# Performance work log

Measured on AMD Instinct MI355X. Metric: run time of the kernel, lower is better.

The kernel has to match this reference:

```python
import jax, jax.numpy as jnp
import numpy as np

HD = 256          # hidden_dim[0]
KF = 2            # k factor
KD = HD * KF      # 512, bilinear feature dim
L = 2000          # hard-coded sequence length
B = 4
NEG = np.float32(np.finfo(np.float32).min)  # finite min, NOT -inf (matches torch code)
EPS = 1e-5


def _fc(x, V, g, b):
    # weight_norm(Linear, dim=None): W = g * V / ||V||_F, then ReLU
    W = (g / jnp.linalg.norm(V)) * V  # [KD, HD]
    return jax.nn.relu(jnp.einsum('blh,kh->blk', x, W) + b)


def setup_inputs() -> dict:
    key = jax.random.key(0)
    ks = jax.random.split(key, 12)
    X = jax.random.normal(ks[0], (B, L, HD), dtype=jnp.float32)
    Y = jax.random.normal(ks[1], (B, L, HD), dtype=jnp.float32)
    mask1 = jax.random.bernoulli(ks[2], 0.8, (B, L)).astype(jnp.float32)
    mask2 = jax.random.bernoulli(ks[3], 0.8, (B, L)).astype(jnp.float32)
    # Q_net / K_net params (single weight-normed linear each)
    Qv = jax.random.normal(ks[4], (KD, HD), dtype=jnp.float32) * 0.05
    Qg = jnp.asarray(1.0, dtype=jnp.float32)
    Qb = jax.random.normal(ks[5], (KD,), dtype=jnp.float32) * 0.05
    Kv = jax.random.normal(ks[6], (KD, HD), dtype=jnp.float32) * 0.05
    Kg = jnp.asarray(1.0, dtype=jnp.float32)
    Kb = jax.random.normal(ks[7], (KD,), dtype=jnp.float32) * 0.05
    h_mat = jax.random.normal(ks[8], (KD,), dtype=jnp.float32)   # (1,1,KD) squeezed
    h_bias = jax.random.normal(ks[9], (), dtype=jnp.float32)     # (1,1,1) squeezed
    gamma = jnp.ones((KD,), dtype=jnp.float32)                   # BatchNorm1d affine
    beta = jnp.zeros((KD,), dtype=jnp.float32)
    return {"X": X, "Y": Y, "mask1": mask1, "mask2": mask2,
            "Qv": Qv, "Qg": Qg, "Qb": Qb, "Kv": Kv, "Kg": Kg, "Kb": Kb,
            "h_mat": h_mat, "h_bias": h_bias, "gamma": gamma, "beta": beta}


def _masked_softmax(A, m_row):
    # m_row: [B,1,L], broadcasts over axis 1; softmax over dim 1 as in torch
    logits = jnp.where(m_row > 0, A, NEG)
    att = jax.nn.softmax(logits, axis=1)
    return m_row * att


def reference(X, Y, mask1, mask2, Qv, Qg, Qb, Kv, Kg, Kb, h_mat, h_bias, gamma, beta):
    A1_X = _fc(X, Qv, Qg, Qb)  # [B,L,KD]
    A1_Y = _fc(Y, Kv, Kg, Kb)
    A2_Y = _fc(Y, Qv, Qg, Qb)
    A2_X = _fc(X, Kv, Kg, Kb)
    # bilinear co-attention maps [B,L,L]
    A1 = jnp.einsum('bvk,bqk->bvq', A1_X * h_mat, A1_Y) + h_bias
    A2 = jnp.einsum('bqk,bvk->bqv', A2_Y * h_mat, A2_X) + h_bias
    m1r = mask1[:, None, :]  # mask1_attend[b,v,q] = mask1[b,q]
    m2r = mask2[:, None, :]
    alpha = _masked_softmax(A1, m2r)
    logits_X = jnp.einsum('bvq,bqk->bvk', alpha, A1_Y) * mask1[:, :, None]
    beta_att = _masked_softmax(A2, m1r)
    logits_Y = jnp.einsum('bqv,bvk->bqk', beta_att, A2_X) * mask2[:, :, None]
    # AvgPool2d((2000,1)) == mean over sequence dim
    pooled = logits_X.mean(axis=1) + logits_Y.mean(axis=1)  # [B,KD]
    # BatchNorm1d training-mode forward (biased batch stats)
    mu = pooled.mean(axis=0)
    var = pooled.var(axis=0)
    return gamma * (pooled - mu) * jax.lax.rsqrt(var + EPS) + beta
```

## Files before the change

kernel.cpp:

```cpp
#include <hip/hip_runtime.h>

#define NB 4
#define LSEQ 2000
#define HD 256
#define KD 512
#define LPAD 2048
#define SMALL_N 18562

using short8 = __attribute__((ext_vector_type(8))) short;
using f32x4  = __attribute__((ext_vector_type(4))) float;
typedef unsigned short u16;

__device__ __forceinline__ float b2f(u16 u) { return __uint_as_float(((unsigned)u) << 16); }
__device__ __forceinline__ u16 f2b(float f) {
    unsigned u = __float_as_uint(f);
    u += 0x7FFFu + ((u >> 16) & 1u);
    return (u16)(u >> 16);
}
__device__ __forceinline__ bool detect32(const void* gamma) {
    return ((const float*)gamma)[0] == 1.0f;
}
__device__ __forceinline__ void gl_lds16(const u16* g, short* l) {
    __builtin_amdgcn_global_load_lds(
        (const __attribute__((address_space(1))) unsigned int*)g,
        (__attribute__((address_space(3))) unsigned int*)l, 16, 0, 0);
}

__global__ void convert_kernel(const void* X, const void* Y, const void* Qv, const void* Kv,
                               const void* m1, const void* m2, const void* Qb, const void* Kb,
                               const void* hm, const void* Qg, const void* Kg,
                               const void* gamma, const void* beta,
                               u16* __restrict__ Xb, u16* __restrict__ Yb,
                               u16* __restrict__ Qvb, u16* __restrict__ Kvb,
                               float* __restrict__ smallf, float* __restrict__ ssq)
{
    const bool is32 = detect32(gamma);
    const int seg = blockIdx.y;
    if (seg < 4) {
        const void* src = seg == 0 ? X : seg == 1 ? Y : seg == 2 ? Qv : Kv;
        u16* dst = seg == 0 ? Xb : seg == 1 ? Yb : seg == 2 ? Qvb : Kvb;
        const int n = (seg < 2) ? NB * LSEQ * HD : KD * HD;
        const int i0 = (blockIdx.x * 256 + threadIdx.x) * 8;
        if (i0 >= n) return;
        uint4 pack;
        u16* v = (u16*)&pack;
        if (is32) {
            float4 fa = ((const float4*)src)[(i0 >> 2)];
            float4 fb = ((const float4*)src)[(i0 >> 2) + 1];
            v[0] = f2b(fa.x); v[1] = f2b(fa.y); v[2] = f2b(fa.z); v[3] = f2b(fa.w);
            v[4] = f2b(fb.x); v[5] = f2b(fb.y); v[6] = f2b(fb.z); v[7] = f2b(fb.w);
        } else {
            pack = ((const uint4*)src)[i0 >> 3];
        }
        ((uint4*)dst)[i0 >> 3] = pack;
        if (seg >= 2) {
            float s = 0.f;
            #pragma unroll
            for (int j = 0; j < 8; ++j) { float f = b2f(v[j]); s = fmaf(f, f, s); }
            #pragma unroll
            for (int off = 32; off > 0; off >>= 1) s += __shfl_xor(s, off);
            if ((threadIdx.x & 63) == 0) atomicAdd(&ssq[seg - 2], s);
        }
    } else {
        const int i0 = (blockIdx.x * 256 + threadIdx.x) * 4;
        for (int i = i0; i < i0 + 4; ++i) {
            if (i >= SMALL_N) break;
            const void* src; int off;
            if      (i <  8000) { src = m1;    off = i; }
            else if (i < 16000) { src = m2;    off = i - 8000; }
            else if (i < 16512) { src = Qb;    off = i - 16000; }
            else if (i < 17024) { src = Kb;    off = i - 16512; }
            else if (i < 17536) { src = hm;    off = i - 17024; }
            else if (i < 18048) { src = gamma; off = i - 17536; }
            else if (i < 18560) { src = beta;  off = i - 18048; }
            else if (i == 18560) {
                float f = ((const float*)Qg)[0];
                smallf[i] = (f == 1.0f) ? 1.0f : b2f(((const u16*)Qg)[0]);
                continue;
            } else {
                float f = ((const float*)Kg)[0];
                smallf[i] = (f == 1.0f) ? 1.0f : b2f(((const u16*)Kg)[0]);
                continue;
            }
            smallf[i] = is32 ? ((const float*)src)[off] : b2f(((const u16*)src)[off]);
        }
    }
}

__global__ __launch_bounds__(256, 2)
void fc_kernel(const u16* __restrict__ X, const u16* __restrict__ Y,
               const u16* __restrict__ Qv, const u16* __restrict__ Kv,
               const float* __restrict__ Qbf, const float* __restrict__ Kbf,
               const float* __restrict__ hf, const float* __restrict__ gv,
               const float* __restrict__ ssq, u16* __restrict__ fc)
{
    const int mt = blockIdx.x, nt = blockIdx.y, t = blockIdx.z;
    const int b = t >> 2, which = t & 3;
    const u16* In = ((which == 0) | (which == 3)) ? (X + (size_t)b * LSEQ * HD)
                                                  : (Y + (size_t)b * LSEQ * HD);
    const bool isQ = (which == 0) | (which == 2);
    const u16* W      = isQ ? Qv : Kv;
    const float* bias = isQ ? Qbf : Kbf;
    const int j = isQ ? 0 : 1;
    const float s = gv[j] / sqrtf(ssq[j]);
    u16* out = fc + (size_t)t * LSEQ * KD;

    __shared__ __align__(16) short As[2][128 * 32];
    __shared__ __align__(16) short Bs[2][128 * 32];

    const int tid = threadIdx.x;
    const int lane = tid & 63, wave = tid >> 6;
    const int wm = wave >> 1, wn = wave & 1;
    const int quad = lane >> 4, l15 = lane & 15;
    const int sr = tid >> 2, sc = tid & 3;
    const int scz = sc ^ ((sr >> 1) & 3);
    const int m0 = mt * 128, n0 = nt * 128;

    int gm0 = min(m0 + sr, LSEQ - 1), gm1 = min(m0 + sr + 64, LSEQ - 1);
    const u16* pA0 = In + (size_t)gm0 * HD + scz * 8;
    const u16* pA1 = In + (size_t)gm1 * HD + scz * 8;
    const u16* pB0 = W + (size_t)(n0 + sr) * HD + scz * 8;
    const u16* pB1 = W + (size_t)(n0 + sr + 64) * HD + scz * 8;
    const int dof = sr * 32 + sc * 8;

    int aoff[4], boff[4];
    #pragma unroll
    for (int i = 0; i < 4; ++i) {
        int ra = wm * 64 + i * 16 + l15;
        aoff[i] = ra * 32 + (quad ^ ((ra >> 1) & 3)) * 8;
        int rb = wn * 64 + i * 16 + l15;
        boff[i] = rb * 32 + (quad ^ ((rb >> 1) & 3)) * 8;
    }

    gl_lds16(pA0, &As[0][dof]);
    gl_lds16(pA1, &As[0][64 * 32 + dof]);
    gl_lds16(pB0, &Bs[0][dof]);
    gl_lds16(pB1, &Bs[0][64 * 32 + dof]);
    __syncthreads();

    f32x4 acc[4][4] = {};

    for (int kt = 0; kt < 8; ++kt) {
        const int cur = kt & 1, nxt = cur ^ 1;
        if (kt < 7) {
            const int ko = (kt + 1) * 32;
            gl_lds16(pA0 + ko, &As[nxt][dof]);
            gl_lds16(pA1 + ko, &As[nxt][64 * 32 + dof]);
            gl_lds16(pB0 + ko, &Bs[nxt][dof]);
            gl_lds16(pB1 + ko, &Bs[nxt][64 * 32 + dof]);
        }
        short8 af[4], bf[4];
        #pragma unroll
        for (int i = 0; i < 4; ++i) af[i] = *(const short8*)&As[cur][aoff[i]];
        #pragma unroll
        for (int i = 0; i < 4; ++i) bf[i] = *(const short8*)&Bs[cur][boff[i]];
        #pragma unroll
        for (int mi = 0; mi < 4; ++mi)
            #pragma unroll
            for (int ni = 0; ni < 4; ++ni)
                acc[mi][ni] = __builtin_amdgcn_mfma_f32_16x16x32_bf16(af[mi], bf[ni], acc[mi][ni], 0, 0, 0);
        __syncthreads();
    }

    #pragma unroll
    for (int ni = 0; ni < 4; ++ni) {
        int n = n0 + wn * 64 + ni * 16 + l15;
        float bv = bias[n];
        float hv = isQ ? hf[n] : 1.0f;
        #pragma unroll
        for (int mi = 0; mi < 4; ++mi) {
            int mb = m0 + wm * 64 + mi * 16 + quad * 4;
            #pragma unroll
            for (int r = 0; r < 4; ++r) {
                int m = mb + r;
                if (m < LSEQ) {
                    float v = fmaf(s, acc[mi][ni][r], bv);
                    v = v > 0.f ? v : 0.f;
                    out[(size_t)m * KD + n] = f2b(v * hv);
                }
            }
        }
    }
}

__global__ __launch_bounds__(256, 2)
void colsm_kernel(const u16* __restrict__ fc, const float* __restrict__ m1f,
                  const float* __restrict__ m2f,
                  float* __restrict__ part_d, float* __restrict__ part_n)
{
    const int vs = blockIdx.x, qt = blockIdx.y, z = blockIdx.z;
    const int a = z >> 2, b = z & 3;
    const u16* R  = fc + (size_t)(b * 4 + (a == 0 ? 1 : 3)) * LSEQ * KD;
    const u16* Sm = fc + (size_t)(b * 4 + (a == 0 ? 0 : 2)) * LSEQ * KD;
    const float* wmask = (a == 0 ? m1f : m2f) + (size_t)b * LSEQ;

    __shared__ __align__(16) short Rs[2][128 * 32];
    __shared__ __align__(16) short Ss[2][128 * 32];
    __shared__ float ldsD[128][2];
    __shared__ float ldsN[128][2];

    const int tid = threadIdx.x;
    const int lane = tid & 63, wave = tid >> 6;
    const int wrow = wave >> 1, wcol = wave & 1;
    const int quad = lane >> 4, l15 = lane & 15;
    const int sr = tid >> 2, sc = tid & 3;
    const int scz = sc ^ ((sr >> 1) & 3);
    const int r0 = qt * 128, c0 = vs * 128;

    int gr0 = min(r0 + sr, LSEQ - 1), gr1 = min(r0 + sr + 64, LSEQ - 1);
    int gc0 = min(c0 + sr, LSEQ - 1), gc1 = min(c0 + sr + 64, LSEQ - 1);
    const u16* pR0 = R  + (size_t)gr0 * KD + scz * 8;
    const u16* pR1 = R  + (size_t)gr1 * KD + scz * 8;
    const u16* pS0 = Sm + (size_t)gc0 * KD + scz * 8;
    const u16* pS1 = Sm + (size_t)gc1 * KD + scz * 8;
    const int dof = sr * 32 + sc * 8;

    int aoff[4], boff[4];
    #pragma unroll
    for (int i = 0; i < 4; ++i) {
        int ra = wrow * 64 + i * 16 + l15;
        aoff[i] = ra * 32 + (quad ^ ((ra >> 1) & 3)) * 8;
        int rb = wcol * 64 + i * 16 + l15;
        boff[i] = rb * 32 + (quad ^ ((rb >> 1) & 3)) * 8;
    }

    gl_lds16(pR0, &Rs[0][dof]);
    gl_lds16(pR1, &Rs[0][64 * 32 + dof]);
    gl_lds16(pS0, &Ss[0][dof]);
    gl_lds16(pS1, &Ss[0][64 * 32 + dof]);
    __syncthreads();

    f32x4 acc[4][4] = {};

    for (int kt = 0; kt < 16; ++kt) {
        const int cur = kt & 1, nxt = cur ^ 1;
        if (kt < 15) {
            const int ko = (kt + 1) * 32;
            gl_lds16(pR0 + ko, &Rs[nxt][dof]);
            gl_lds16(pR1 + ko, &Rs[nxt][64 * 32 + dof]);
            gl_lds16(pS0 + ko, &Ss[nxt][dof]);
            gl_lds16(pS1 + ko, &Ss[nxt][64 * 32 + dof]);
        }
        short8 af[4], bf[4];
        #pragma unroll
        for (int i = 0; i < 4; ++i) af[i] = *(const short8*)&Rs[cur][aoff[i]];
        #pragma unroll
        for (int i = 0; i < 4; ++i) bf[i] = *(const short8*)&Ss[cur][boff[i]];
        #pragma unroll
        for (int mi = 0; mi < 4; ++mi)
            #pragma unroll
            for (int ni = 0; ni < 4; ++ni)
                acc[mi][ni] = __builtin_amdgcn_mfma_f32_16x16x32_bf16(af[mi], bf[ni], acc[mi][ni], 0, 0, 0);
        __syncthreads();
    }

    float wv[4], vv[4];
    #pragma unroll
    for (int ni = 0; ni < 4; ++ni) {
        int cg = c0 + wcol * 64 + ni * 16 + l15;
        bool valid = cg < LSEQ;
        vv[ni] = valid ? 1.f : 0.f;
        wv[ni] = valid ? wmask[cg] : 0.f;
    }
    #pragma unroll
    for (int mi = 0; mi < 4; ++mi)
        #pragma unroll
        for (int r = 0; r < 4; ++r) {
            float d = 0.f, n = 0.f;
            #pragma unroll
            for (int ni = 0; ni < 4; ++ni) {
                float e = __expf(acc[mi][ni][r]);
                d = fmaf(vv[ni], e, d);
                n = fmaf(wv[ni], e, n);
            }
            #pragma unroll
            for (int off = 1; off < 16; off <<= 1) {
                d += __shfl_xor(d, off);
                n += __shfl_xor(n, off);
            }
            if (l15 == 0) {
                int row = wrow * 64 + mi * 16 + quad * 4 + r;
                ldsD[row][wcol] = d;
                ldsN[row][wcol] = n;
            }
        }
    __syncthreads();
    if (tid < 128) {
        int q = r0 + tid;
        if (q < LSEQ) {
            size_t p = ((size_t)(z * 16 + vs)) * LPAD + q;
            part_d[p] = ldsD[tid][0] + ldsD[tid][1];
            part_n[p] = ldsN[tid][0] + ldsN[tid][1];
        }
    }
}

__global__ void combine_kernel(const float* __restrict__ part_d, const float* __restrict__ part_n,
                               const float* __restrict__ m1f, const float* __restrict__ m2f,
                               float* __restrict__ c, float* __restrict__ pooled)
{
    int idx = blockIdx.x * 256 + threadIdx.x;
    if (idx < NB * KD) pooled[idx] = 0.f;
    int z = idx >> 11, q = idx & (LPAD - 1);
    int a = z >> 2, b = z & 3;
    float d = 0.f, n = 0.f;
    #pragma unroll
    for (int vs = 0; vs < 16; ++vs) {
        size_t p = ((size_t)(z * 16 + vs)) * LPAD + q;
        d += part_d[p]; n += part_n[p];
    }
    float val = 0.f;
    if (q < LSEQ) {
        float om = (a == 0 ? m2f : m1f)[b * LSEQ + q];
        val = om * n / d;
    }
    c[(size_t)z * LPAD + q] = val;
}

__global__ void pooled_kernel(const u16* __restrict__ fc, const float* __restrict__ c,
                              float* __restrict__ pooled)
{
    const int b = blockIdx.x, rs = blockIdx.y;
    const int k = threadIdx.x;
    const u16* YK = fc + (size_t)(b * 4 + 1) * LSEQ * KD;
    const u16* XK = fc + (size_t)(b * 4 + 3) * LSEQ * KD;
    const float* c1 = c + (size_t)(0 + b) * LPAD;
    const float* c2 = c + (size_t)(4 + b) * LPAD;
    float s = 0.f;
    const int rbeg = rs * 50, rend = rbeg + 50;
    for (int r = rbeg; r < rend; ++r) {
        s = fmaf(c1[r], b2f(YK[(size_t)r * KD + k]), s);
        s = fmaf(c2[r], b2f(XK[(size_t)r * KD + k]), s);
    }
    atomicAdd(&pooled[b * KD + k], s * (1.0f / LSEQ));
}

__global__ void ln_kernel(const float* __restrict__ pooled, const float* __restrict__ gammaf,
                          const float* __restrict__ betaf, const void* __restrict__ gamma_orig,
                          void* __restrict__ out)
{
    int k = blockIdx.x * 256 + threadIdx.x;
    float p[NB];
    #pragma unroll
    for (int b = 0; b < NB; ++b) p[b] = pooled[b * KD + k];
    float mu = 0.25f * (p[0] + p[1] + p[2] + p[3]);
    float var = 0.f;
    #pragma unroll
    for (int b = 0; b < NB; ++b) { float d = p[b] - mu; var = fmaf(d, d, var); }
    var *= 0.25f;
    float inv = rsqrtf(var + 1e-5f);
    float g = gammaf[k], be = betaf[k];
    const bool is32 = detect32(gamma_orig);
    #pragma unroll
    for (int b = 0; b < NB; ++b) {
        float v = fmaf(g * (p[b] - mu), inv, be);
        if (is32) ((float*)out)[b * KD + k] = v;
        else      ((u16*)out)[b * KD + k] = f2b(v);
    }
}

extern "C" void kernel_launch(void* const* d_in, const int* in_sizes, int n_in,
                              void* d_out, int out_size, void* d_ws, size_t ws_size,
                              hipStream_t stream)
{
    const void* X  = d_in[0];
    const void* Y  = d_in[1];
    const void* m1 = d_in[2];
    const void* m2 = d_in[3];
    const void* Qv = d_in[4];
    const void* Qg = d_in[5];
    const void* Qb = d_in[6];
    const void* Kv = d_in[7];
    const void* Kg = d_in[8];
    const void* Kb = d_in[9];
    const void* h  = d_in[10];
    const void* gamma = d_in[12];
    const void* beta  = d_in[13];

    char* ws = (char*)d_ws;
    size_t off = 0;
    u16* Xb  = (u16*)(ws + off); off += (size_t)NB * LSEQ * HD * 2;
    u16* Yb  = (u16*)(ws + off); off += (size_t)NB * LSEQ * HD * 2;
    u16* Qvb = (u16*)(ws + off); off += (size_t)KD * HD * 2;
    u16* Kvb = (u16*)(ws + off); off += (size_t)KD * HD * 2;
    float* smallf = (float*)(ws + off); off += ((size_t)(SMALL_N + 2) * 4 + 15) / 16 * 16;
    u16* fc  = (u16*)(ws + off); off += (size_t)16 * LSEQ * KD * 2;
    float* part_d = (float*)(ws + off); off += (size_t)8 * 16 * LPAD * 4;
    float* part_n = (float*)(ws + off); off += (size_t)8 * 16 * LPAD * 4;
    float* c      = (float*)(ws + off); off += (size_t)8 * LPAD * 4;
    float* pooled = (float*)(ws + off); off += (size_t)NB * KD * 4;

    const float* m1f = smallf;
    const float* m2f = smallf + 8000;
    const float* Qbf = smallf + 16000;
    const float* Kbf = smallf + 16512;
    const float* hf  = smallf + 17024;
    const float* gmf = smallf + 17536;
    const float* bef = smallf + 18048;
    const float* gv  = smallf + 18560;
    float* ssq = smallf + SMALL_N;

    hipMemsetAsync(ssq, 0, 2 * sizeof(float), stream);
    convert_kernel<<<dim3(1000, 5), 256, 0, stream>>>(X, Y, Qv, Kv, m1, m2, Qb, Kb, h, Qg, Kg,
                                                      gamma, beta, Xb, Yb, Qvb, Kvb, smallf, ssq);
    fc_kernel     <<<dim3(16, 4, 16), 256, 0, stream>>>(Xb, Yb, Qvb, Kvb, Qbf, Kbf, hf, gv, ssq, fc);
    colsm_kernel  <<<dim3(16, 16, 8), 256, 0, stream>>>(fc, m1f, m2f, part_d, part_n);
    combine_kernel<<<64, 256, 0, stream>>>(part_d, part_n, m1f, m2f, c, pooled);
    pooled_kernel <<<dim3(4, 40), 512, 0, stream>>>(fc, c, pooled);
    ln_kernel     <<<2, 256, 0, stream>>>(pooled, gmf, bef, gamma, d_out);
}
```

Before: 197.1 us.

## Triple-buffer LDS tiles with one barrier per k-step and MFMA priority

Both GEMM kernels (fc and column-softmax) switch from double to triple-buffered LDS staging. Loads run two k-steps ahead, guarded by explicit vmcnt waits and a single barrier per iteration instead of two syncthreads. The k loop is unrolled and s_setprio raises wave priority around the MFMA block. This adds LDS per block (48KB for the tiles), which could affect the two-blocks-per-CU occupancy target, and relies on hand-counted vmcnt values being correct.

```diff
diff --git a/kernel.cpp b/kernel.cpp
--- a/kernel.cpp
+++ b/kernel.cpp
@@ -105,8 +105,8 @@
     const float s = gv[j] / sqrtf(ssq[j]);
     u16* out = fc + (size_t)t * LSEQ * KD;
 
-    __shared__ __align__(16) short As[2][128 * 32];
-    __shared__ __align__(16) short Bs[2][128 * 32];
+    __shared__ __align__(16) short As[3][128 * 32];
+    __shared__ __align__(16) short Bs[3][128 * 32];
 
     const int tid = threadIdx.x;
     const int lane = tid & 63, wave = tid >> 6;
@@ -136,30 +136,43 @@
     gl_lds16(pA1, &As[0][64 * 32 + dof]);
     gl_lds16(pB0, &Bs[0][dof]);
     gl_lds16(pB1, &Bs[0][64 * 32 + dof]);
-    __syncthreads();
+    gl_lds16(pA0 + 32, &As[1][dof]);
+    gl_lds16(pA1 + 32, &As[1][64 * 32 + dof]);
+    gl_lds16(pB0 + 32, &Bs[1][dof]);
+    gl_lds16(pB1 + 32, &Bs[1][64 * 32 + dof]);
 
     f32x4 acc[4][4] = {};
 
+    #pragma unroll
     for (int kt = 0; kt < 8; ++kt) {
-        const int cur = kt & 1, nxt = cur ^ 1;
-        if (kt < 7) {
-            const int ko = (kt + 1) * 32;
-            gl_lds16(pA0 + ko, &As[nxt][dof]);
-            gl_lds16(pA1 + ko, &As[nxt][64 * 32 + dof]);
-            gl_lds16(pB0 + ko, &Bs[nxt][dof]);
-            gl_lds16(pB1 + ko, &Bs[nxt][64 * 32 + dof]);
-        }
+        if (kt >= 6) asm volatile("s_waitcnt vmcnt(0)" ::: "memory");
+        else         asm volatile("s_waitcnt vmcnt(4)" ::: "memory");
+        __builtin_amdgcn_s_barrier();
+        asm volatile("" ::: "memory");
+        __builtin_amdgcn_sched_barrier(0);
+        if (kt < 6) {
+            const int ko = (kt + 2) * 32;
+            short* An = As[(kt + 2) % 3];
+            short* Bn = Bs[(kt + 2) % 3];
+            gl_lds16(pA0 + ko, &An[dof]);
+            gl_lds16(pA1 + ko, &An[64 * 32 + dof]);
+            gl_lds16(pB0 + ko, &Bn[dof]);
+            gl_lds16(pB1 + ko, &Bn[64 * 32 + dof]);
+        }
+        const short* Ac = As[kt % 3];
+        const short* Bc = Bs[kt % 3];
         short8 af[4], bf[4];
         #pragma unroll
-        for (int i = 0; i < 4; ++i) af[i] = *(const short8*)&As[cur][aoff[i]];
-        #pragma unroll
-        for (int i = 0; i < 4; ++i) bf[i] = *(const short8*)&Bs[cur][boff[i]];
+        for (int i = 0; i < 4; ++i) af[i] = *(const short8*)&Ac[aoff[i]];
+        #pragma unroll
+        for (int i = 0; i < 4; ++i) bf[i] = *(const short8*)&Bc[boff[i]];
+        __builtin_amdgcn_s_setprio(1);
         #pragma unroll
         for (int mi = 0; mi < 4; ++mi)
             #pragma unroll
             for (int ni = 0; ni < 4; ++ni)
                 acc[mi][ni] = __builtin_amdgcn_mfma_f32_16x16x32_bf16(af[mi], bf[ni], acc[mi][ni], 0, 0, 0);
-        __syncthreads();
+        __builtin_amdgcn_s_setprio(0);
     }
 
     #pragma unroll
@@ -194,8 +207,8 @@
     const u16* Sm = fc + (size_t)(b * 4 + (a == 0 ? 0 : 2)) * LSEQ * KD;
     const float* wmask = (a == 0 ? m1f : m2f) + (size_t)b * LSEQ;
 
-    __shared__ __align__(16) short Rs[2][128 * 32];
-    __shared__ __align__(16) short Ss[2][128 * 32];
+    __shared__ __align__(16) short Rs[3][128 * 32];
+    __shared__ __align__(16) short Ss[3][128 * 32];
     __shared__ float ldsD[128][2];
     __shared__ float ldsN[128][2];
 
@@ -228,30 +241,43 @@
     gl_lds16(pR1, &Rs[0][64 * 32 + dof]);
     gl_lds16(pS0, &Ss[0][dof]);
     gl_lds16(pS1, &Ss[0][64 * 32 + dof]);
-    __syncthreads();
+    gl_lds16(pR0 + 32, &Rs[1][dof]);
+    gl_lds16(pR1 + 32, &Rs[1][64 * 32 + dof]);
+    gl_lds16(pS0 + 32, &Ss[1][dof]);
+    gl_lds16(pS1 + 32, &Ss[1][64 * 32 + dof]);
 
     f32x4 acc[4][4] = {};
 
+    #pragma unroll
     for (int kt = 0; kt < 16; ++kt) {
-        const int cur = kt & 1, nxt = cur ^ 1;
-        if (kt < 15) {
-            const int ko = (kt + 1) * 32;
-            gl_lds16(pR0 + ko, &Rs[nxt][dof]);
-            gl_lds16(pR1 + ko, &Rs[nxt][64 * 32 + dof]);
-            gl_lds16(pS0 + ko, &Ss[nxt][dof]);
-            gl_lds16(pS1 + ko, &Ss[nxt][64 * 32 + dof]);
-        }
+        if (kt >= 14) asm volatile("s_waitcnt vmcnt(0)" ::: "memory");
+        else          asm volatile("s_waitcnt vmcnt(4)" ::: "memory");
+        __builtin_amdgcn_s_barrier();
+        asm volatile("" ::: "memory");
+        __builtin_amdgcn_sched_barrier(0);
+        if (kt < 14) {
+            const int ko = (kt + 2) * 32;
+            short* Rn = Rs[(kt + 2) % 3];
+            short* Sn = Ss[(kt + 2) % 3];
+            gl_lds16(pR0 + ko, &Rn[dof]);
+            gl_lds16(pR1 + ko, &Rn[64 * 32 + dof]);
+            gl_lds16(pS0 + ko, &Sn[dof]);
+            gl_lds16(pS1 + ko, &Sn[64 * 32 + dof]);
+        }
+        const short* Rc = Rs[kt % 3];
+        const short* Sc = Ss[kt % 3];
         short8 af[4], bf[4];
         #pragma unroll
-        for (int i = 0; i < 4; ++i) af[i] = *(const short8*)&Rs[cur][aoff[i]];
-        #pragma unroll
-        for (int i = 0; i < 4; ++i) bf[i] = *(const short8*)&Ss[cur][boff[i]];
+        for (int i = 0; i < 4; ++i) af[i] = *(const short8*)&Rc[aoff[i]];
+        #pragma unroll
+        for (int i = 0; i < 4; ++i) bf[i] = *(const short8*)&Sc[boff[i]];
+        __builtin_amdgcn_s_setprio(1);
         #pragma unroll
         for (int mi = 0; mi < 4; ++mi)
             #pragma unroll
             for (int ni = 0; ni < 4; ++ni)
                 acc[mi][ni] = __builtin_amdgcn_mfma_f32_16x16x32_bf16(af[mi], bf[ni], acc[mi][ni], 0, 0, 0);
-        __syncthreads();
+        __builtin_amdgcn_s_setprio(0);
     }
 
     float wv[4], vv[4];
```

Measured after the change: 202.1 us. +2.5%, slower.

## Enlarge colsm tiles to 256x256 with 4-stage LDS pipeline and ping-pong barriers

Applied to the files above, without the earlier changes.

The score-plus-exp-sum kernel now uses 512-thread blocks computing 256x256 tiles instead of 128x128, with eight waves each owning 128x64 outputs. Global-to-LDS staging becomes a four-deep ring buffer with explicit vmcnt waits, and MFMA phases are wrapped in barriers and raised priority to interleave loads with compute. Larger tiles halve operand reloads per output and halve the partial-sum count that combine_kernel reduces. The trade-off is higher LDS use (128KB) and register pressure, and fewer blocks (512) to fill the GPU.

```diff
diff --git a/kernel.cpp b/kernel.cpp
--- a/kernel.cpp
+++ b/kernel.cpp
@@ -183,7 +183,7 @@
     }
 }
 
-__global__ __launch_bounds__(256, 2)
+__global__ __launch_bounds__(512, 2)
 void colsm_kernel(const u16* __restrict__ fc, const float* __restrict__ m1f,
                   const float* __restrict__ m2f,
                   float* __restrict__ part_d, float* __restrict__ part_n)
@@ -194,82 +194,108 @@
     const u16* Sm = fc + (size_t)(b * 4 + (a == 0 ? 0 : 2)) * LSEQ * KD;
     const float* wmask = (a == 0 ? m1f : m2f) + (size_t)b * LSEQ;
 
-    __shared__ __align__(16) short Rs[2][128 * 32];
-    __shared__ __align__(16) short Ss[2][128 * 32];
-    __shared__ float ldsD[128][2];
-    __shared__ float ldsN[128][2];
+    __shared__ __align__(16) short AL[4][256 * 32];
+    __shared__ __align__(16) short BL[4][256 * 32];
 
     const int tid = threadIdx.x;
     const int lane = tid & 63, wave = tid >> 6;
-    const int wrow = wave >> 1, wcol = wave & 1;
+    const int wm = wave >> 2, wn = wave & 3;
     const int quad = lane >> 4, l15 = lane & 15;
-    const int sr = tid >> 2, sc = tid & 3;
-    const int scz = sc ^ ((sr >> 1) & 3);
-    const int r0 = qt * 128, c0 = vs * 128;
-
-    int gr0 = min(r0 + sr, LSEQ - 1), gr1 = min(r0 + sr + 64, LSEQ - 1);
-    int gc0 = min(c0 + sr, LSEQ - 1), gc1 = min(c0 + sr + 64, LSEQ - 1);
-    const u16* pR0 = R  + (size_t)gr0 * KD + scz * 8;
-    const u16* pR1 = R  + (size_t)gr1 * KD + scz * 8;
-    const u16* pS0 = Sm + (size_t)gc0 * KD + scz * 8;
-    const u16* pS1 = Sm + (size_t)gc1 * KD + scz * 8;
-    const int dof = sr * 32 + sc * 8;
-
-    int aoff[4], boff[4];
-    #pragma unroll
-    for (int i = 0; i < 4; ++i) {
-        int ra = wrow * 64 + i * 16 + l15;
-        aoff[i] = ra * 32 + (quad ^ ((ra >> 1) & 3)) * 8;
-        int rb = wcol * 64 + i * 16 + l15;
-        boff[i] = rb * 32 + (quad ^ ((rb >> 1) & 3)) * 8;
-    }
-
-    gl_lds16(pR0, &Rs[0][dof]);
-    gl_lds16(pR1, &Rs[0][64 * 32 + dof]);
-    gl_lds16(pS0, &Ss[0][dof]);
-    gl_lds16(pS1, &Ss[0][64 * 32 + dof]);
+    const int r0 = qt * 256, c0 = vs * 256;
+
+    const int srow = tid >> 2;
+    const int kslot = (tid & 3) ^ ((tid >> 3) & 3);
+    int grA0 = min(r0 + srow, LSEQ - 1), grA1 = min(r0 + 128 + srow, LSEQ - 1);
+    int gcB0 = min(c0 + srow, LSEQ - 1), gcB1 = min(c0 + 128 + srow, LSEQ - 1);
+    const u16* pRa = R  + (size_t)grA0 * KD + kslot * 8;
+    const u16* pRb = R  + (size_t)grA1 * KD + kslot * 8;
+    const u16* pSa = Sm + (size_t)gcB0 * KD + kslot * 8;
+    const u16* pSb = Sm + (size_t)gcB1 * KD + kslot * 8;
+    const int ldst = tid * 8;
+
+    const int swz = (quad ^ ((l15 >> 1) & 3)) * 8;
+
+    #define STAGE_A(h) { short* d_ = &AL[(h) & 3][ldst];               \
+                         gl_lds16(pRa + (h) * 32, d_);                 \
+                         gl_lds16(pRb + (h) * 32, d_ + 4096); }
+    #define STAGE_B(h) { short* d_ = &BL[(h) & 3][ldst];               \
+                         gl_lds16(pSa + (h) * 32, d_);                 \
+                         gl_lds16(pSb + (h) * 32, d_ + 4096); }
+
+    STAGE_A(0); STAGE_B(0); STAGE_A(1); STAGE_B(1); STAGE_A(2); STAGE_B(2);
+    asm volatile("s_waitcnt vmcnt(4)" ::: "memory");
+    __builtin_amdgcn_s_barrier();
+    __builtin_amdgcn_sched_barrier(0);
+
+    f32x4 acc[8][4] = {};
+    short8 bf[4];
+
+    #pragma unroll 2
+    for (int t = 0; t < 8; ++t) {
+        #pragma unroll
+        for (int p = 0; p < 4; ++p) {
+            const int j = 2 * t + (p >> 1);
+            const short* Ab = AL[j & 3];
+            const short* Bb = BL[j & 3];
+            short8 af[4];
+            #pragma unroll
+            for (int mi = 0; mi < 4; ++mi) {
+                int lr = wm * 128 + (p & 1) * 64 + mi * 16 + l15;
+                af[mi] = *(const short8*)&Ab[lr * 32 + swz];
+            }
+            if ((p & 1) == 0) {
+                #pragma unroll
+                for (int ni = 0; ni < 4; ++ni) {
+                    int lc = wn * 64 + ni * 16 + l15;
+                    bf[ni] = *(const short8*)&Bb[lc * 32 + swz];
+                }
+            }
+            if (p == 0)      { if (2 * t + 3 <= 15) STAGE_A(2 * t + 3); }
+            else if (p == 1) { if (2 * t + 3 <= 15) STAGE_B(2 * t + 3); }
+            else if (p == 2) { if (2 * t + 4 <= 15) STAGE_A(2 * t + 4); }
+            else {
+                if (2 * t + 4 <= 15) STAGE_B(2 * t + 4);
+                if (t < 6)       asm volatile("s_waitcnt vmcnt(4)" ::: "memory");
+                else if (t == 6) asm volatile("s_waitcnt vmcnt(0)" ::: "memory");
+            }
+            asm volatile("" ::: "memory");
+            __builtin_amdgcn_s_barrier();
+            __builtin_amdgcn_sched_barrier(0);
+            __builtin_amdgcn_s_setprio(1);
+            #pragma unroll
+            for (int mi = 0; mi < 4; ++mi)
+                #pragma unroll
+                for (int ni = 0; ni < 4; ++ni)
+                    acc[(p & 1) * 4 + mi][ni] =
+                        __builtin_amdgcn_mfma_f32_16x16x32_bf16(af[mi], bf[ni],
+                                                                acc[(p & 1) * 4 + mi][ni], 0, 0, 0);
+            __builtin_amdgcn_s_setprio(0);
+            asm volatile("" ::: "memory");
+            __builtin_amdgcn_s_barrier();
+            __builtin_amdgcn_sched_barrier(0);
+        }
+    }
+
     __syncthreads();
-
-    f32x4 acc[4][4] = {};
-
-    for (int kt = 0; kt < 16; ++kt) {
-        const int cur = kt & 1, nxt = cur ^ 1;
-        if (kt < 15) {
-            const int ko = (kt + 1) * 32;
-            gl_lds16(pR0 + ko, &Rs[nxt][dof]);
-            gl_lds16(pR1 + ko, &Rs[nxt][64 * 32 + dof]);
-            gl_lds16(pS0 + ko, &Ss[nxt][dof]);
-            gl_lds16(pS1 + ko, &Ss[nxt][64 * 32 + dof]);
-        }
-        short8 af[4], bf[4];
-        #pragma unroll
-        for (int i = 0; i < 4; ++i) af[i] = *(const short8*)&Rs[cur][aoff[i]];
-        #pragma unroll
-        for (int i = 0; i < 4; ++i) bf[i] = *(const short8*)&Ss[cur][boff[i]];
-        #pragma unroll
-        for (int mi = 0; mi < 4; ++mi)
-            #pragma unroll
-            for (int ni = 0; ni < 4; ++ni)
-                acc[mi][ni] = __builtin_amdgcn_mfma_f32_16x16x32_bf16(af[mi], bf[ni], acc[mi][ni], 0, 0, 0);
-        __syncthreads();
-    }
+    float* ldsD = (float*)&AL[0][0];
+    float* ldsN = (float*)&AL[1][0];
 
     float wv[4], vv[4];
     #pragma unroll
     for (int ni = 0; ni < 4; ++ni) {
-        int cg = c0 + wcol * 64 + ni * 16 + l15;
+        int cg = c0 + wn * 64 + ni * 16 + l15;
         bool valid = cg < LSEQ;
         vv[ni] = valid ? 1.f : 0.f;
-        wv[ni] = valid ? wmask[cg] : 0.f;
-    }
-    #pragma unroll
-    for (int mi = 0; mi < 4; ++mi)
+        wv[ni] = valid ? wmask[min(cg, LSEQ - 1)] : 0.f;
+    }
+    #pragma unroll
+    for (int aq = 0; aq < 8; ++aq)
         #pragma unroll
         for (int r = 0; r < 4; ++r) {
             float d = 0.f, n = 0.f;
             #pragma unroll
             for (int ni = 0; ni < 4; ++ni) {
-                float e = __expf(acc[mi][ni][r]);
+                float e = __expf(acc[aq][ni][r]);
                 d = fmaf(vv[ni], e, d);
                 n = fmaf(wv[ni], e, n);
             }
@@ -279,20 +305,22 @@
                 n += __shfl_xor(n, off);
             }
             if (l15 == 0) {
-                int row = wrow * 64 + mi * 16 + quad * 4 + r;
-                ldsD[row][wcol] = d;
-                ldsN[row][wcol] = n;
+                int row = wm * 128 + (aq >> 2) * 64 + (aq & 3) * 16 + quad * 4 + r;
+                ldsD[row * 4 + wn] = d;
+                ldsN[row * 4 + wn] = n;
             }
         }
     __syncthreads();
-    if (tid < 128) {
+    if (tid < 256) {
         int q = r0 + tid;
         if (q < LSEQ) {
-            size_t p = ((size_t)(z * 16 + vs)) * LPAD + q;
-            part_d[p] = ldsD[tid][0] + ldsD[tid][1];
-            part_n[p] = ldsN[tid][0] + ldsN[tid][1];
-        }
-    }
+            size_t p = ((size_t)(z * 8 + vs)) * LPAD + q;
+            part_d[p] = ldsD[tid * 4 + 0] + ldsD[tid * 4 + 1] + ldsD[tid * 4 + 2] + ldsD[tid * 4 + 3];
+            part_n[p] = ldsN[tid * 4 + 0] + ldsN[tid * 4 + 1] + ldsN[tid * 4 + 2] + ldsN[tid * 4 + 3];
+        }
+    }
+    #undef STAGE_A
+    #undef STAGE_B
 }
 
 __global__ void combine_kernel(const float* __restrict__ part_d, const float* __restrict__ part_n,
@@ -305,8 +333,8 @@
     int a = z >> 2, b = z & 3;
     float d = 0.f, n = 0.f;
     #pragma unroll
-    for (int vs = 0; vs < 16; ++vs) {
-        size_t p = ((size_t)(z * 16 + vs)) * LPAD + q;
+    for (int vs = 0; vs < 8; ++vs) {
+        size_t p = ((size_t)(z * 8 + vs)) * LPAD + q;
         d += part_d[p]; n += part_n[p];
     }
     float val = 0.f;
@@ -385,8 +413,8 @@
     u16* Kvb = (u16*)(ws + off); off += (size_t)KD * HD * 2;
     float* smallf = (float*)(ws + off); off += ((size_t)(SMALL_N + 2) * 4 + 15) / 16 * 16;
     u16* fc  = (u16*)(ws + off); off += (size_t)16 * LSEQ * KD * 2;
-    float* part_d = (float*)(ws + off); off += (size_t)8 * 16 * LPAD * 4;
-    float* part_n = (float*)(ws + off); off += (size_t)8 * 16 * LPAD * 4;
+    float* part_d = (float*)(ws + off); off += (size_t)8 * 8 * LPAD * 4;
+    float* part_n = (float*)(ws + off); off += (size_t)8 * 8 * LPAD * 4;
     float* c      = (float*)(ws + off); off += (size_t)8 * LPAD * 4;
     float* pooled = (float*)(ws + off); off += (size_t)NB * KD * 4;
 
@@ -404,7 +432,7 @@
     convert_kernel<<<dim3(1000, 5), 256, 0, stream>>>(X, Y, Qv, Kv, m1, m2, Qb, Kb, h, Qg, Kg,
                                                       gamma, beta, Xb, Yb, Qvb, Kvb, smallf, ssq);
     fc_kernel     <<<dim3(16, 4, 16), 256, 0, stream>>>(Xb, Yb, Qvb, Kvb, Qbf, Kbf, hf, gv, ssq, fc);
-    colsm_kernel  <<<dim3(16, 16, 8), 256, 0, stream>>>(fc, m1f, m2f, part_d, part_n);
+    colsm_kernel  <<<dim3(8, 8, 8), 512, 0, stream>>>(fc, m1f, m2f, part_d, part_n);
     combine_kernel<<<64, 256, 0, stream>>>(part_d, part_n, m1f, m2f, c, pooled);
     pooled_kernel <<<dim3(4, 40), 512, 0, stream>>>(fc, c, pooled);
     ln_kernel     <<<2, 256, 0, stream>>>(pooled, gmf, bef, gamma, d_out);
```

After: 193.4 us. No clear change (-1.9%).
